# Kernel tuning notes

Hardware: AMD Instinct MI355X
Metric: run time of the kernel (lower is better)

## Reference

```python
import jax, jax.numpy as jnp
import numpy as np

B, S, HID = 1, 2048, 4096
NH, NKV, HD = 32, 8, 128
BLOCK, NBLOCKS = 64, 64
NUSED = S // BLOCK  # 32 blocks hold the sequence
SCALE = HD ** -0.5


def setup_inputs() -> dict:
    key = jax.random.key(0)
    ks = jax.random.split(key, 8)
    hidden_states = jax.random.normal(ks[0], (B, S, HID), jnp.float32)
    # RoPE tables (Llama-style)
    inv_freq = 1.0 / (10000.0 ** (np.arange(0, HD, 2, dtype=np.float32) / HD))
    freqs = np.outer(np.arange(S, dtype=np.float32), inv_freq)  # [S, HD/2]
    emb = np.concatenate([freqs, freqs], axis=-1)               # [S, HD]
    cos = jnp.asarray(np.cos(emb), jnp.float32)[None]           # [1, S, HD]
    sin = jnp.asarray(np.sin(emb), jnp.float32)[None]
    wq = jax.random.normal(ks[1], (NH * HD, HID), jnp.float32) * 0.02
    wk = jax.random.normal(ks[2], (NKV * HD, HID), jnp.float32) * 0.02
    wv = jax.random.normal(ks[3], (NKV * HD, HID), jnp.float32) * 0.02
    wo = jax.random.normal(ks[4], (HID, NH * HD), jnp.float32) * 0.02
    k_cache = jnp.zeros((NBLOCKS, NKV, BLOCK, HD), jnp.float32)
    v_cache = jnp.zeros((NBLOCKS, NKV, BLOCK, HD), jnp.float32)
    # irregular (non-contiguous) block allocation, like a paged KV cache
    block_ids = jax.random.permutation(ks[5], NBLOCKS)[:NUSED].astype(jnp.int32)
    return {"hidden_states": hidden_states, "cos": cos, "sin": sin,
            "wq": wq, "wk": wk, "wv": wv, "wo": wo,
            "k_cache": k_cache, "v_cache": v_cache, "block_ids": block_ids}


def _rotate_half(x):
    x1, x2 = x[..., : HD // 2], x[..., HD // 2:]
    return jnp.concatenate([-x2, x1], axis=-1)


def reference(hidden_states, cos, sin, wq, wk, wv, wo, k_cache, v_cache, block_ids):
    # QKV projections (no bias per attention_bias=False)
    q = jnp.einsum('bsh,dh->bsd', hidden_states, wq).reshape(B, S, NH, HD).transpose(0, 2, 1, 3)   # [B,NH,S,HD]
    k = jnp.einsum('bsh,dh->bsd', hidden_states, wk).reshape(B, S, NKV, HD).transpose(0, 2, 1, 3)  # [B,NKV,S,HD]
    v = jnp.einsum('bsh,dh->bsd', hidden_states, wv).reshape(B, S, NKV, HD).transpose(0, 2, 1, 3)

    # --- paged KV cache: scatter new K/V into non-contiguous blocks (append_kv) ---
    kb = k[0].reshape(NKV, NUSED, BLOCK, HD).transpose(1, 0, 2, 3)  # [NUSED,NKV,BLOCK,HD]
    vb = v[0].reshape(NKV, NUSED, BLOCK, HD).transpose(1, 0, 2, 3)
    k_cache = k_cache.at[block_ids].set(kb)
    v_cache = v_cache.at[block_ids].set(vb)
    # --- gather cached KV back across block list (get_cached_kv) ---
    kg = k_cache[block_ids].transpose(1, 0, 2, 3).reshape(NKV, S, HD)[None]  # [1,NKV,S,HD]
    vg = v_cache[block_ids].transpose(1, 0, 2, 3).reshape(NKV, S, HD)[None]

    # RoPE on q and gathered k
    c, s = cos[:, None], sin[:, None]  # [1,1,S,HD]
    q = q * c + _rotate_half(q) * s
    kg = kg * c + _rotate_half(kg) * s

    # GQA: repeat KV heads
    kr = jnp.repeat(kg, NH // NKV, axis=1)  # [1,NH,S,HD]
    vr = jnp.repeat(vg, NH // NKV, axis=1)

    scores = jnp.einsum('bhqd,bhkd->bhqk', q, kr) * SCALE
    causal = jnp.arange(S)[:, None] >= jnp.arange(S)[None, :]
    scores = jnp.where(causal, scores, jnp.finfo(scores.dtype).min)
    attn = jax.nn.softmax(scores, axis=-1)
    out = jnp.einsum('bhqk,bhkd->bhqd', attn, vr)
    out = out.transpose(0, 2, 1, 3).reshape(B, S, NH * HD)
    return jnp.einsum('bsd,hd->bsh', out, wo)
```

## Files before the change

### kernel.cpp

```cpp
#include <hip/hip_runtime.h>
#include <hip/hip_bf16.h>
#include <stdint.h>

#define SEQ 2048
#define HIDDEN 4096
#define NHEAD 32
#define NKVH 8
#define HDIM 128
#define NQT (SEQ / 64)
#define SCALE 0.08838834764831845f

typedef __bf16 bf16x8 __attribute__((ext_vector_type(8)));
typedef float floatx4 __attribute__((ext_vector_type(4)));

__device__ inline float bf2f(unsigned int u16) {
    union { unsigned int i; float f; } x;
    x.i = u16 << 16;
    return x.f;
}
__device__ inline unsigned short f2bf(float f) {
    union { float f; unsigned int u; } x;
    x.f = f;
    unsigned int r = x.u + 0x7FFF + ((x.u >> 16) & 1);
    return (unsigned short)(r >> 16);
}

__global__ __launch_bounds__(256) void cast_f32_bf16(const float* __restrict__ s,
                                                     unsigned short* __restrict__ d, int n4) {
    int i = blockIdx.x * 256 + threadIdx.x;
    if (i < n4) {
        float4 v = ((const float4*)s)[i];
        ushort4 o;
        o.x = f2bf(v.x); o.y = f2bf(v.y); o.z = f2bf(v.z); o.w = f2bf(v.w);
        ((ushort4*)d)[i] = o;
    }
}

__device__ inline void storeC(float* p, float v) { *p = v; }
__device__ inline void storeC(unsigned short* p, float v) { *p = f2bf(v); }

#define GLL16(gp, lp) __builtin_amdgcn_global_load_lds( \
    (const __attribute__((address_space(1))) unsigned int*)(gp), \
    (__attribute__((address_space(3))) unsigned int*)(lp), 16, 0, 0)

template <typename OutT, bool TRANSOUT = false>
__global__ __launch_bounds__(256) void gemm_nt_mfma(const unsigned short* __restrict__ A,
                                                    const unsigned short* __restrict__ B,
                                                    OutT* __restrict__ C,
                                                    int M, int N, int K) {
    __shared__ unsigned short As[128 * 32];
    __shared__ unsigned short Bs[128 * 32];
    const int tid = threadIdx.x;
    const int lane = tid & 63;
    const int w = tid >> 6;
    const int m0 = blockIdx.y * 128, n0 = blockIdx.x * 128;
    const int wr = (w >> 1) * 64, wc = (w & 1) * 64;
    const int srow = tid >> 2;
    const int scol = (tid & 3) * 8;
    const int quad = lane >> 4, l16 = lane & 15;

    floatx4 acc[4][4] = {};

    for (int k0 = 0; k0 < K; k0 += 32) {
        __syncthreads();
        const unsigned short* gA = A + (size_t)(m0 + srow) * K + k0 + scol;
        const unsigned short* gB = B + (size_t)(n0 + srow) * K + k0 + scol;
        GLL16(gA,                  As + srow * 32 + scol);
        GLL16(gA + (size_t)64 * K, As + (64 + srow) * 32 + scol);
        GLL16(gB,                  Bs + srow * 32 + scol);
        GLL16(gB + (size_t)64 * K, Bs + (64 + srow) * 32 + scol);
        __syncthreads();

        bf16x8 af[4], bg[4];
        #pragma unroll
        for (int i = 0; i < 4; ++i)
            af[i] = *(const bf16x8*)(As + (wr + i * 16 + l16) * 32 + quad * 8);
        #pragma unroll
        for (int j = 0; j < 4; ++j)
            bg[j] = *(const bf16x8*)(Bs + (wc + j * 16 + l16) * 32 + quad * 8);
        #pragma unroll
        for (int i = 0; i < 4; ++i)
            #pragma unroll
            for (int j = 0; j < 4; ++j)
                acc[i][j] = __builtin_amdgcn_mfma_f32_16x16x32_bf16(af[i], bg[j], acc[i][j], 0, 0, 0);
    }

    #pragma unroll
    for (int i = 0; i < 4; ++i) {
        #pragma unroll
        for (int j = 0; j < 4; ++j) {
            int col = n0 + wc + j * 16 + l16;
            int rowb = m0 + wr + i * 16 + quad * 4;
            if constexpr (TRANSOUT) {
                ushort4 pk;
                pk.x = f2bf(acc[i][j][0]);
                pk.y = f2bf(acc[i][j][1]);
                pk.z = f2bf(acc[i][j][2]);
                pk.w = f2bf(acc[i][j][3]);
                *(ushort4*)&C[(size_t)col * M + rowb] = pk;
            } else {
                #pragma unroll
                for (int r = 0; r < 4; ++r)
                    storeC(&C[(size_t)(rowb + r) * N + col], acc[i][j][r]);
            }
        }
    }
}

__global__ __launch_bounds__(256) void gemm_kv_mfma(const unsigned short* __restrict__ A,
                                                    const unsigned short* __restrict__ B,
                                                    unsigned short* __restrict__ Ck,
                                                    unsigned short* __restrict__ Cvt) {
    const int M = SEQ, K = HIDDEN;
    __shared__ unsigned short As[128 * 32];
    __shared__ unsigned short Bs[128 * 32];
    const int tid = threadIdx.x;
    const int lane = tid & 63;
    const int w = tid >> 6;
    const int m0 = blockIdx.y * 128, n0 = blockIdx.x * 128;
    const int wr = (w >> 1) * 64, wc = (w & 1) * 64;
    const int srow = tid >> 2;
    const int scol = (tid & 3) * 8;
    const int quad = lane >> 4, l16 = lane & 15;

    floatx4 acc[4][4] = {};

    for (int k0 = 0; k0 < K; k0 += 32) {
        __syncthreads();
        const unsigned short* gA = A + (size_t)(m0 + srow) * K + k0 + scol;
        const unsigned short* gB = B + (size_t)(n0 + srow) * K + k0 + scol;
        GLL16(gA,                  As + srow * 32 + scol);
        GLL16(gA + (size_t)64 * K, As + (64 + srow) * 32 + scol);
        GLL16(gB,                  Bs + srow * 32 + scol);
        GLL16(gB + (size_t)64 * K, Bs + (64 + srow) * 32 + scol);
        __syncthreads();

        bf16x8 af[4], bg[4];
        #pragma unroll
        for (int i = 0; i < 4; ++i)
            af[i] = *(const bf16x8*)(As + (wr + i * 16 + l16) * 32 + quad * 8);
        #pragma unroll
        for (int j = 0; j < 4; ++j)
            bg[j] = *(const bf16x8*)(Bs + (wc + j * 16 + l16) * 32 + quad * 8);
        #pragma unroll
        for (int i = 0; i < 4; ++i)
            #pragma unroll
            for (int j = 0; j < 4; ++j)
                acc[i][j] = __builtin_amdgcn_mfma_f32_16x16x32_bf16(af[i], bg[j], acc[i][j], 0, 0, 0);
    }

    if (n0 < NKVH * HDIM) {
        const int N = NKVH * HDIM;
        #pragma unroll
        for (int i = 0; i < 4; ++i) {
            #pragma unroll
            for (int j = 0; j < 4; ++j) {
                int col = n0 + wc + j * 16 + l16;
                int rowb = m0 + wr + i * 16 + quad * 4;
                #pragma unroll
                for (int r = 0; r < 4; ++r)
                    Ck[(size_t)(rowb + r) * N + col] = f2bf(acc[i][j][r]);
            }
        }
    } else {
        #pragma unroll
        for (int i = 0; i < 4; ++i) {
            #pragma unroll
            for (int j = 0; j < 4; ++j) {
                int col = n0 - NKVH * HDIM + wc + j * 16 + l16;
                int rowb = m0 + wr + i * 16 + quad * 4;
                ushort4 pk;
                pk.x = f2bf(acc[i][j][0]);
                pk.y = f2bf(acc[i][j][1]);
                pk.z = f2bf(acc[i][j][2]);
                pk.w = f2bf(acc[i][j][3]);
                *(ushort4*)&Cvt[(size_t)col * M + rowb] = pk;
            }
        }
    }
}

__global__ __launch_bounds__(256) void rope_bf16(unsigned short* __restrict__ x,
                                                 const float* __restrict__ cosb,
                                                 const float* __restrict__ sinb,
                                                 int nh) {
    int idx = blockIdx.x * 256 + threadIdx.x;
    int d = idx & 63;
    int t = idx >> 6;
    int h = t % nh;
    int s = t / nh;
    float cs = cosb[s * HDIM + d];
    float sn = sinb[s * HDIM + d];
    unsigned short* p = x + (size_t)s * nh * HDIM + h * HDIM + d;
    float x1 = bf2f(p[0]), x2 = bf2f(p[64]);
    p[0]  = f2bf(x1 * cs - x2 * sn);
    p[64] = f2bf(x2 * cs + x1 * sn);
}

__global__ __launch_bounds__(256) void attn_mfma(const unsigned short* __restrict__ qg,
                                                 const unsigned short* __restrict__ kgb,
                                                 const unsigned short* __restrict__ vtg,
                                                 unsigned short* __restrict__ ao) {
    __shared__ unsigned short Ks[2][64 * 128];
    __shared__ unsigned short Vs[2][128 * 64];
    __shared__ unsigned short Ps[4][16 * 64];
    const int h = blockIdx.y;
    const int kvh = h >> 2;
    const int tid = threadIdx.x;
    const int w = tid >> 6, lane = tid & 63;
    const int quad = lane >> 4, l16 = lane & 15;
    const int srow16 = tid >> 4, sc16 = tid & 15;
    const int sdim8 = tid >> 3, skc8 = tid & 7;

    auto stage = [&](int buf, int t) {
        #pragma unroll
        for (int rl = 0; rl < 4; ++rl) {
            int key = rl * 16 + srow16;
            int cg = sc16 ^ (key & 7);
            const unsigned short* gp = kgb + (size_t)(t * 64 + key) * (NKVH * HDIM) + kvh * HDIM + cg * 8;
            GLL16(gp, &Ks[buf][key * 128 + sc16 * 8]);
        }
        #pragma unroll
        for (int rl = 0; rl < 4; ++rl) {
            int dim = rl * 32 + sdim8;
            int kg2 = skc8 ^ (dim & 7);
            const unsigned short* gp = vtg + (size_t)(kvh * HDIM + dim) * SEQ + t * 64 + kg2 * 8;
            GLL16(gp, &Vs[buf][dim * 64 + skc8 * 8]);
        }
    };

    #pragma unroll 1
    for (int ph = 0; ph < 2; ++ph) {
        const int qt = ph ? (NQT - 1 - (int)blockIdx.x) : (int)blockIdx.x;
        const int s0 = qt * 64;

        bf16x8 aq[4];
        {
            const unsigned short* qrowp = qg + (size_t)(s0 + w * 16 + l16) * (NHEAD * HDIM) + h * HDIM;
            #pragma unroll
            for (int ks = 0; ks < 4; ++ks)
                aq[ks] = *(const bf16x8*)(qrowp + ks * 32 + quad * 8);
        }

        floatx4 acc_o[8] = {};
        float m_r[4], l_r[4];
        #pragma unroll
        for (int r = 0; r < 4; ++r) { m_r[r] = -1e30f; l_r[r] = 0.f; }

        stage(0, 0);
        __syncthreads();
        int cur = 0;

        for (int t = 0; t <= qt; ++t) {
            if (t < qt) stage(cur ^ 1, t + 1);
            const unsigned short* Kc = &Ks[cur][0];
            const unsigned short* Vc = &Vs[cur][0];

            floatx4 acc_s[4] = {};
            #pragma unroll
            for (int ks = 0; ks < 4; ++ks)
                #pragma unroll
                for (int jt = 0; jt < 4; ++jt) {
                    bf16x8 bk = *(const bf16x8*)(Kc + (jt * 16 + l16) * 128 +
                                                 (((ks * 4 + quad) ^ (l16 & 7)) * 8));
                    acc_s[jt] = __builtin_amdgcn_mfma_f32_16x16x32_bf16(aq[ks], bk, acc_s[jt], 0, 0, 0);
                }

            float s_v[4][4];
            #pragma unroll
            for (int jt = 0; jt < 4; ++jt)
                #pragma unroll
                for (int r = 0; r < 4; ++r)
                    s_v[jt][r] = acc_s[jt][r] * SCALE;
            if (t == qt) {
                #pragma unroll
                for (int jt = 0; jt < 4; ++jt) {
                    int key = t * 64 + jt * 16 + l16;
                    #pragma unroll
                    for (int r = 0; r < 4; ++r) {
                        int qrow = s0 + w * 16 + quad * 4 + r;
                        if (key > qrow) s_v[jt][r] = -1e30f;
                    }
                }
            }

            float p_v[4][4];
            #pragma unroll
            for (int r = 0; r < 4; ++r) {
                float v = fmaxf(fmaxf(s_v[0][r], s_v[1][r]), fmaxf(s_v[2][r], s_v[3][r]));
                #pragma unroll
                for (int off = 1; off < 16; off <<= 1) v = fmaxf(v, __shfl_xor(v, off));
                float mn = fmaxf(m_r[r], v);
                float alpha = __expf(m_r[r] - mn);
                m_r[r] = mn;
                float sum = 0.f;
                #pragma unroll
                for (int jt = 0; jt < 4; ++jt) { p_v[jt][r] = __expf(s_v[jt][r] - mn); sum += p_v[jt][r]; }
                #pragma unroll
                for (int off = 1; off < 16; off <<= 1) sum += __shfl_xor(sum, off);
                l_r[r] = l_r[r] * alpha + sum;
                #pragma unroll
                for (int nt = 0; nt < 8; ++nt) acc_o[nt][r] *= alpha;
            }

            unsigned short* pw = Ps[w];
            #pragma unroll
            for (int jt = 0; jt < 4; ++jt)
                #pragma unroll
                for (int r = 0; r < 4; ++r) {
                    int row = quad * 4 + r;
                    int c = (2 * jt + (l16 >> 3)) ^ (row & 7);
                    pw[row * 64 + c * 8 + (l16 & 7)] = f2bf(p_v[jt][r]);
                }
            #pragma unroll
            for (int ks = 0; ks < 2; ++ks) {
                bf16x8 ap = *(const bf16x8*)(pw + l16 * 64 + (((ks * 4 + quad) ^ (l16 & 7)) * 8));
                #pragma unroll
                for (int nt = 0; nt < 8; ++nt) {
                    bf16x8 bv = *(const bf16x8*)(Vc + (nt * 16 + l16) * 64 +
                                                 (((ks * 4 + quad) ^ (l16 & 7)) * 8));
                    acc_o[nt] = __builtin_amdgcn_mfma_f32_16x16x32_bf16(ap, bv, acc_o[nt], 0, 0, 0);
                }
            }

            __syncthreads();
            cur ^= 1;
        }

        #pragma unroll
        for (int r = 0; r < 4; ++r) {
            float inv = 1.f / l_r[r];
            int qrow = s0 + w * 16 + quad * 4 + r;
            unsigned short* op = ao + (size_t)qrow * (NHEAD * HDIM) + h * HDIM + l16;
            #pragma unroll
            for (int nt = 0; nt < 8; ++nt)
                op[nt * 16] = f2bf(acc_o[nt][r] * inv);
        }
    }
}

extern "C" void kernel_launch(void* const* d_in, const int* in_sizes, int n_in,
                              void* d_out, int out_size, void* d_ws, size_t ws_size,
                              hipStream_t stream) {
    const float* hidden = (const float*)d_in[0];
    const float* cosb   = (const float*)d_in[1];
    const float* sinb   = (const float*)d_in[2];
    const float* wq     = (const float*)d_in[3];
    const float* wk     = (const float*)d_in[4];
    const float* wv     = (const float*)d_in[5];
    const float* wo     = (const float*)d_in[6];

    unsigned short* hb  = (unsigned short*)d_ws;
    unsigned short* wb  = hb + (size_t)SEQ * HIDDEN;
    unsigned short* qb  = wb + (size_t)HIDDEN * HIDDEN;
    unsigned short* kb  = qb + (size_t)SEQ * NHEAD * HDIM;
    unsigned short* vtb = kb + (size_t)SEQ * NKVH * HDIM;
    unsigned short* ao  = hb;

    dim3 blk(256);
    cast_f32_bf16<<<dim3(SEQ * HIDDEN / 1024), blk, 0, stream>>>(hidden, hb, SEQ * HIDDEN / 4);

    cast_f32_bf16<<<dim3(HIDDEN * HIDDEN / 1024), blk, 0, stream>>>(wq, wb, HIDDEN * HIDDEN / 4);
    gemm_nt_mfma<unsigned short><<<dim3((NHEAD * HDIM) / 128, SEQ / 128), blk, 0, stream>>>(
        hb, wb, qb, SEQ, NHEAD * HDIM, HIDDEN);

    cast_f32_bf16<<<dim3(NKVH * HDIM * HIDDEN / 1024), blk, 0, stream>>>(wk, wb, NKVH * HDIM * HIDDEN / 4);
    cast_f32_bf16<<<dim3(NKVH * HDIM * HIDDEN / 1024), blk, 0, stream>>>(
        wv, wb + (size_t)(NKVH * HDIM) * HIDDEN, NKVH * HDIM * HIDDEN / 4);
    gemm_kv_mfma<<<dim3((2 * NKVH * HDIM) / 128, SEQ / 128), blk, 0, stream>>>(hb, wb, kb, vtb);

    rope_bf16<<<dim3(SEQ * NHEAD * 64 / 256), blk, 0, stream>>>(qb, cosb, sinb, NHEAD);
    rope_bf16<<<dim3(SEQ * NKVH * 64 / 256), blk, 0, stream>>>(kb, cosb, sinb, NKVH);

    attn_mfma<<<dim3(NQT / 2, NHEAD), blk, 0, stream>>>(qb, kb, vtb, ao);

    cast_f32_bf16<<<dim3(HIDDEN * HIDDEN / 1024), blk, 0, stream>>>(wo, wb, HIDDEN * HIDDEN / 4);
    gemm_nt_mfma<float><<<dim3(HIDDEN / 128, SEQ / 128), blk, 0, stream>>>(
        ao, wb, (float*)d_out, SEQ, HIDDEN, NHEAD * HDIM);
}
```

Baseline: 623.2 us.

## Double-buffer GEMM LDS tiles and fuse Q/K/V projections into one GEMM

Both GEMM kernels now use two LDS buffers and prefetch the next K-slice with global_load_lds while running MFMAs on the current slice. This drops one barrier per iteration and hides global load latency. The Q and KV projection GEMMs are merged into a single launch over a concatenated bf16 weight buffer, with outputs routed to Q, K or transposed V depending on column range. This fills the GPU with one larger grid. LDS use doubles per block, which may lower occupancy, and there is a possible race: the prefetch writes into the other buffer without an explicit wait for its async loads before the barrier.

```diff
diff --git a/kernel.cpp b/kernel.cpp
--- a/kernel.cpp
+++ b/kernel.cpp
@@ -43,13 +43,13 @@
     (const __attribute__((address_space(1))) unsigned int*)(gp), \
     (__attribute__((address_space(3))) unsigned int*)(lp), 16, 0, 0)
 
-template <typename OutT, bool TRANSOUT = false>
+template <typename OutT>
 __global__ __launch_bounds__(256) void gemm_nt_mfma(const unsigned short* __restrict__ A,
                                                     const unsigned short* __restrict__ B,
                                                     OutT* __restrict__ C,
                                                     int M, int N, int K) {
-    __shared__ unsigned short As[128 * 32];
-    __shared__ unsigned short Bs[128 * 32];
+    __shared__ unsigned short As[2][128 * 32];
+    __shared__ unsigned short Bs[2][128 * 32];
     const int tid = threadIdx.x;
     const int lane = tid & 63;
     const int w = tid >> 6;
@@ -59,30 +59,39 @@
     const int scol = (tid & 3) * 8;
     const int quad = lane >> 4, l16 = lane & 15;
 
-    floatx4 acc[4][4] = {};
-
-    for (int k0 = 0; k0 < K; k0 += 32) {
-        __syncthreads();
+    auto stage = [&](int buf, int k0) {
         const unsigned short* gA = A + (size_t)(m0 + srow) * K + k0 + scol;
         const unsigned short* gB = B + (size_t)(n0 + srow) * K + k0 + scol;
-        GLL16(gA,                  As + srow * 32 + scol);
-        GLL16(gA + (size_t)64 * K, As + (64 + srow) * 32 + scol);
-        GLL16(gB,                  Bs + srow * 32 + scol);
-        GLL16(gB + (size_t)64 * K, Bs + (64 + srow) * 32 + scol);
-        __syncthreads();
+        GLL16(gA,                  &As[buf][srow * 32 + scol]);
+        GLL16(gA + (size_t)64 * K, &As[buf][(64 + srow) * 32 + scol]);
+        GLL16(gB,                  &Bs[buf][srow * 32 + scol]);
+        GLL16(gB + (size_t)64 * K, &Bs[buf][(64 + srow) * 32 + scol]);
+    };
+
+    floatx4 acc[4][4] = {};
+
+    stage(0, 0);
+    __syncthreads();
+    int cur = 0;
+
+    for (int k0 = 0; k0 < K; k0 += 32) {
+        if (k0 + 32 < K) stage(cur ^ 1, k0 + 32);
 
         bf16x8 af[4], bg[4];
         #pragma unroll
         for (int i = 0; i < 4; ++i)
-            af[i] = *(const bf16x8*)(As + (wr + i * 16 + l16) * 32 + quad * 8);
+            af[i] = *(const bf16x8*)(&As[cur][(wr + i * 16 + l16) * 32 + quad * 8]);
         #pragma unroll
         for (int j = 0; j < 4; ++j)
-            bg[j] = *(const bf16x8*)(Bs + (wc + j * 16 + l16) * 32 + quad * 8);
+            bg[j] = *(const bf16x8*)(&Bs[cur][(wc + j * 16 + l16) * 32 + quad * 8]);
         #pragma unroll
         for (int i = 0; i < 4; ++i)
             #pragma unroll
             for (int j = 0; j < 4; ++j)
                 acc[i][j] = __builtin_amdgcn_mfma_f32_16x16x32_bf16(af[i], bg[j], acc[i][j], 0, 0, 0);
+
+        __syncthreads();
+        cur ^= 1;
     }
 
     #pragma unroll
@@ -91,29 +100,21 @@
         for (int j = 0; j < 4; ++j) {
             int col = n0 + wc + j * 16 + l16;
             int rowb = m0 + wr + i * 16 + quad * 4;
-            if constexpr (TRANSOUT) {
-                ushort4 pk;
-                pk.x = f2bf(acc[i][j][0]);
-                pk.y = f2bf(acc[i][j][1]);
-                pk.z = f2bf(acc[i][j][2]);
-                pk.w = f2bf(acc[i][j][3]);
-                *(ushort4*)&C[(size_t)col * M + rowb] = pk;
-            } else {
-                #pragma unroll
-                for (int r = 0; r < 4; ++r)
-                    storeC(&C[(size_t)(rowb + r) * N + col], acc[i][j][r]);
-            }
-        }
-    }
-}
-
-__global__ __launch_bounds__(256) void gemm_kv_mfma(const unsigned short* __restrict__ A,
-                                                    const unsigned short* __restrict__ B,
-                                                    unsigned short* __restrict__ Ck,
-                                                    unsigned short* __restrict__ Cvt) {
+            #pragma unroll
+            for (int r = 0; r < 4; ++r)
+                storeC(&C[(size_t)(rowb + r) * N + col], acc[i][j][r]);
+        }
+    }
+}
+
+__global__ __launch_bounds__(256) void gemm_qkv_mfma(const unsigned short* __restrict__ A,
+                                                     const unsigned short* __restrict__ B,
+                                                     unsigned short* __restrict__ Cq,
+                                                     unsigned short* __restrict__ Ck,
+                                                     unsigned short* __restrict__ Cvt) {
     const int M = SEQ, K = HIDDEN;
-    __shared__ unsigned short As[128 * 32];
-    __shared__ unsigned short Bs[128 * 32];
+    __shared__ unsigned short As[2][128 * 32];
+    __shared__ unsigned short Bs[2][128 * 32];
     const int tid = threadIdx.x;
     const int lane = tid & 63;
     const int w = tid >> 6;
@@ -123,51 +124,71 @@
     const int scol = (tid & 3) * 8;
     const int quad = lane >> 4, l16 = lane & 15;
 
-    floatx4 acc[4][4] = {};
-
-    for (int k0 = 0; k0 < K; k0 += 32) {
-        __syncthreads();
+    auto stage = [&](int buf, int k0) {
         const unsigned short* gA = A + (size_t)(m0 + srow) * K + k0 + scol;
         const unsigned short* gB = B + (size_t)(n0 + srow) * K + k0 + scol;
-        GLL16(gA,                  As + srow * 32 + scol);
-        GLL16(gA + (size_t)64 * K, As + (64 + srow) * 32 + scol);
-        GLL16(gB,                  Bs + srow * 32 + scol);
-        GLL16(gB + (size_t)64 * K, Bs + (64 + srow) * 32 + scol);
-        __syncthreads();
+        GLL16(gA,                  &As[buf][srow * 32 + scol]);
+        GLL16(gA + (size_t)64 * K, &As[buf][(64 + srow) * 32 + scol]);
+        GLL16(gB,                  &Bs[buf][srow * 32 + scol]);
+        GLL16(gB + (size_t)64 * K, &Bs[buf][(64 + srow) * 32 + scol]);
+    };
+
+    floatx4 acc[4][4] = {};
+
+    stage(0, 0);
+    __syncthreads();
+    int cur = 0;
+
+    for (int k0 = 0; k0 < K; k0 += 32) {
+        if (k0 + 32 < K) stage(cur ^ 1, k0 + 32);
 
         bf16x8 af[4], bg[4];
         #pragma unroll
         for (int i = 0; i < 4; ++i)
-            af[i] = *(const bf16x8*)(As + (wr + i * 16 + l16) * 32 + quad * 8);
+            af[i] = *(const bf16x8*)(&As[cur][(wr + i * 16 + l16) * 32 + quad * 8]);
         #pragma unroll
         for (int j = 0; j < 4; ++j)
-            bg[j] = *(const bf16x8*)(Bs + (wc + j * 16 + l16) * 32 + quad * 8);
+            bg[j] = *(const bf16x8*)(&Bs[cur][(wc + j * 16 + l16) * 32 + quad * 8]);
         #pragma unroll
         for (int i = 0; i < 4; ++i)
             #pragma unroll
             for (int j = 0; j < 4; ++j)
                 acc[i][j] = __builtin_amdgcn_mfma_f32_16x16x32_bf16(af[i], bg[j], acc[i][j], 0, 0, 0);
-    }
-
-    if (n0 < NKVH * HDIM) {
-        const int N = NKVH * HDIM;
-        #pragma unroll
-        for (int i = 0; i < 4; ++i) {
+
+        __syncthreads();
+        cur ^= 1;
+    }
+
+    if (n0 < NHEAD * HDIM) {
+        const int N = NHEAD * HDIM;
+        #pragma unroll
+        for (int i = 0; i < 4; ++i)
             #pragma unroll
             for (int j = 0; j < 4; ++j) {
                 int col = n0 + wc + j * 16 + l16;
                 int rowb = m0 + wr + i * 16 + quad * 4;
                 #pragma unroll
                 for (int r = 0; r < 4; ++r)
+                    Cq[(size_t)(rowb + r) * N + col] = f2bf(acc[i][j][r]);
+            }
+    } else if (n0 < NHEAD * HDIM + NKVH * HDIM) {
+        const int N = NKVH * HDIM;
+        #pragma unroll
+        for (int i = 0; i < 4; ++i)
+            #pragma unroll
+            for (int j = 0; j < 4; ++j) {
+                int col = n0 - NHEAD * HDIM + wc + j * 16 + l16;
+                int rowb = m0 + wr + i * 16 + quad * 4;
+                #pragma unroll
+                for (int r = 0; r < 4; ++r)
                     Ck[(size_t)(rowb + r) * N + col] = f2bf(acc[i][j][r]);
             }
-        }
     } else {
         #pragma unroll
-        for (int i = 0; i < 4; ++i) {
+        for (int i = 0; i < 4; ++i)
             #pragma unroll
             for (int j = 0; j < 4; ++j) {
-                int col = n0 - NKVH * HDIM + wc + j * 16 + l16;
+                int col = n0 - (NHEAD * HDIM + NKVH * HDIM) + wc + j * 16 + l16;
                 int rowb = m0 + wr + i * 16 + quad * 4;
                 ushort4 pk;
                 pk.x = f2bf(acc[i][j][0]);
@@ -176,7 +197,6 @@
                 pk.w = f2bf(acc[i][j][3]);
                 *(ushort4*)&Cvt[(size_t)col * M + rowb] = pk;
             }
-        }
     }
 }
 
@@ -350,31 +370,31 @@
     const float* wv     = (const float*)d_in[5];
     const float* wo     = (const float*)d_in[6];
 
-    unsigned short* hb  = (unsigned short*)d_ws;
-    unsigned short* wb  = hb + (size_t)SEQ * HIDDEN;
-    unsigned short* qb  = wb + (size_t)HIDDEN * HIDDEN;
-    unsigned short* kb  = qb + (size_t)SEQ * NHEAD * HDIM;
-    unsigned short* vtb = kb + (size_t)SEQ * NKVH * HDIM;
-    unsigned short* ao  = hb;
+    unsigned short* hb   = (unsigned short*)d_ws;
+    unsigned short* wqkv = hb + (size_t)SEQ * HIDDEN;
+    unsigned short* qb   = wqkv + (size_t)(NHEAD + 2 * NKVH) * HDIM * HIDDEN;
+    unsigned short* kb   = qb + (size_t)SEQ * NHEAD * HDIM;
+    unsigned short* vtb  = kb + (size_t)SEQ * NKVH * HDIM;
+    unsigned short* ao   = hb;
 
     dim3 blk(256);
     cast_f32_bf16<<<dim3(SEQ * HIDDEN / 1024), blk, 0, stream>>>(hidden, hb, SEQ * HIDDEN / 4);
 
-    cast_f32_bf16<<<dim3(HIDDEN * HIDDEN / 1024), blk, 0, stream>>>(wq, wb, HIDDEN * HIDDEN / 4);
-    gemm_nt_mfma<unsigned short><<<dim3((NHEAD * HDIM) / 128, SEQ / 128), blk, 0, stream>>>(
-        hb, wb, qb, SEQ, NHEAD * HDIM, HIDDEN);
-
-    cast_f32_bf16<<<dim3(NKVH * HDIM * HIDDEN / 1024), blk, 0, stream>>>(wk, wb, NKVH * HDIM * HIDDEN / 4);
+    cast_f32_bf16<<<dim3(HIDDEN * HIDDEN / 1024), blk, 0, stream>>>(wq, wqkv, HIDDEN * HIDDEN / 4);
     cast_f32_bf16<<<dim3(NKVH * HDIM * HIDDEN / 1024), blk, 0, stream>>>(
-        wv, wb + (size_t)(NKVH * HDIM) * HIDDEN, NKVH * HDIM * HIDDEN / 4);
-    gemm_kv_mfma<<<dim3((2 * NKVH * HDIM) / 128, SEQ / 128), blk, 0, stream>>>(hb, wb, kb, vtb);
+        wk, wqkv + (size_t)NHEAD * HDIM * HIDDEN, NKVH * HDIM * HIDDEN / 4);
+    cast_f32_bf16<<<dim3(NKVH * HDIM * HIDDEN / 1024), blk, 0, stream>>>(
+        wv, wqkv + (size_t)(NHEAD + NKVH) * HDIM * HIDDEN, NKVH * HDIM * HIDDEN / 4);
+
+    gemm_qkv_mfma<<<dim3((NHEAD + 2 * NKVH) * HDIM / 128, SEQ / 128), blk, 0, stream>>>(
+        hb, wqkv, qb, kb, vtb);
 
     rope_bf16<<<dim3(SEQ * NHEAD * 64 / 256), blk, 0, stream>>>(qb, cosb, sinb, NHEAD);
     rope_bf16<<<dim3(SEQ * NKVH * 64 / 256), blk, 0, stream>>>(kb, cosb, sinb, NKVH);
 
     attn_mfma<<<dim3(NQT / 2, NHEAD), blk, 0, stream>>>(qb, kb, vtb, ao);
 
-    cast_f32_bf16<<<dim3(HIDDEN * HIDDEN / 1024), blk, 0, stream>>>(wo, wb, HIDDEN * HIDDEN / 4);
+    cast_f32_bf16<<<dim3(HIDDEN * HIDDEN / 1024), blk, 0, stream>>>(wo, wqkv, HIDDEN * HIDDEN / 4);
     gemm_nt_mfma<float><<<dim3(HIDDEN / 128, SEQ / 128), blk, 0, stream>>>(
-        ao, wb, (float*)d_out, SEQ, HIDDEN, NHEAD * HDIM);
-}
+        ao, wqkv, (float*)d_out, SEQ, HIDDEN, NHEAD * HDIM);
+}
```

Measured after the change: 552.7 us. -11.3%, faster.
